# Optimization experiments

Hardware: AMD Instinct MI355X
Metric: run time of the kernel (lower is better)

## Reference

```python
import jax, jax.numpy as jnp
import numpy as np

N = 2048
DIM = 1024
NH = 16
DK = DIM // NH  # 64

def setup_inputs() -> dict:
    key = jax.random.key(0)
    kx, kq, kk, kv = jax.random.split(key, 4)
    # nn.Linear(dim_in, dim_in, bias=False): init ~ U(-1/sqrt(dim_in), 1/sqrt(dim_in))
    b = 1.0 / np.sqrt(DIM)
    return {
        "x": jax.random.normal(kx, (N, DIM), dtype=jnp.float32),
        "rela": jnp.zeros((1,), dtype=jnp.float32),  # unused by the module
        "Wq": jax.random.uniform(kq, (DIM, DIM), jnp.float32, -b, b),
        "Wk": jax.random.uniform(kk, (DIM, DIM), jnp.float32, -b, b),
        "Wv": jax.random.uniform(kv, (DIM, DIM), jnp.float32, -b, b),
    }

def reference(x, rela, Wq, Wk, Wv):
    n = x.shape[0]
    scale = 1.0 / np.sqrt(DK)
    # torch Linear: x @ W.T ; reshape to [n, nh, dk] then heads first -> [nh, n, dk]
    q = (x @ Wq.T).reshape(n, NH, DK).transpose(1, 0, 2)
    k = (x @ Wk.T).reshape(n, NH, DK).transpose(1, 0, 2)
    v = (x @ Wv.T).reshape(n, NH, DK).transpose(1, 0, 2)
    dist = jnp.einsum('hnd,hmd->hnm', q, k) * scale  # [nh, n, n]
    dist = jax.nn.softmax(dist, axis=-1)
    att = jnp.einsum('hnm,hmd->hnd', dist, v)        # [nh, n, dk]
    return att.transpose(1, 0, 2).reshape(n, DIM)
```

## Files before the change

### kernel.cpp

```cpp
#include <hip/hip_runtime.h>

#define SN 2048
#define SDIM 1024
#define SNH 16
#define SDK 64

typedef short short8 __attribute__((ext_vector_type(8)));
typedef short s16x4 __attribute__((ext_vector_type(4)));
typedef unsigned short u16;
typedef u16 u16x4 __attribute__((ext_vector_type(4)));
typedef float f32x4 __attribute__((ext_vector_type(4)));

__device__ __forceinline__ u16 f2b(float f){
  unsigned u = __builtin_bit_cast(unsigned, f);
  u += 0x7fffu + ((u >> 16) & 1u);
  return (u16)(u >> 16);
}

__device__ __forceinline__ float b2f(u16 b){
  unsigned u = ((unsigned)b) << 16;
  return __builtin_bit_cast(float, u);
}

__device__ __forceinline__ float fast_exp2(float x){
#if __has_builtin(__builtin_amdgcn_exp2f)
  return __builtin_amdgcn_exp2f(x);
#else
  float r; asm("v_exp_f32 %0, %1" : "=v"(r) : "v"(x)); return r;
#endif
}

__device__ __forceinline__ f32x4 mfma16(s16x4 a, s16x4 b, f32x4 c){
#if __has_builtin(__builtin_amdgcn_mfma_f32_16x16x16_bf16)
  return __builtin_amdgcn_mfma_f32_16x16x16_bf16(a, b, c, 0, 0, 0);
#elif __has_builtin(__builtin_amdgcn_mfma_f32_16x16x16bf16_1k)
  return __builtin_amdgcn_mfma_f32_16x16x16bf16_1k(a, b, c, 0, 0, 0);
#else
  asm volatile("v_mfma_f32_16x16x16_bf16 %0, %1, %2, %0" : "+v"(c) : "v"(a), "v"(b));
  return c;
#endif
}

__device__ __forceinline__ void async_cp16(const void* g, void* l){
  __builtin_amdgcn_global_load_lds(
      (const __attribute__((address_space(1))) unsigned*)g,
      (__attribute__((address_space(3))) unsigned*)l, 16, 0, 0);
}

__global__ void conv_all(const float* __restrict__ x, const float* __restrict__ wq,
                         const float* __restrict__ wk, const float* __restrict__ wv,
                         u16* __restrict__ xb, u16* __restrict__ wb){
  const int NX4 = (SN * SDIM) / 4;
  const int NW4 = (SDIM * SDIM) / 4;
  const int total = NX4 + 3 * NW4;
  int i = blockIdx.x * blockDim.x + threadIdx.x;
  int stride = gridDim.x * blockDim.x;
  for (int idx = i; idx < total; idx += stride){
    const float* src; u16* dst; int off;
    if (idx < NX4){ src = x; dst = xb; off = idx; }
    else {
      int t = idx - NX4; int ws = t >> 18; off = t & (NW4 - 1);
      src = (ws == 0) ? wq : ((ws == 1) ? wk : wv);
      dst = wb + (size_t)ws * SDIM * SDIM;
    }
    float4 v = reinterpret_cast<const float4*>(src)[off];
    u16x4 o = { f2b(v.x), f2b(v.y), f2b(v.z), f2b(v.w) };
    *reinterpret_cast<u16x4*>(&dst[(size_t)off * 4]) = o;
  }
}

__global__ __launch_bounds__(256) void proj_gemm(const u16* __restrict__ xb, const u16* __restrict__ wb,
                                                 u16* __restrict__ qb, u16* __restrict__ kb,
                                                 u16* __restrict__ vtb){
  __shared__ __align__(16) u16 Asm[2][64 * 64];
  __shared__ __align__(16) u16 Bsm[2][128 * 64];
  const int tid = threadIdx.x, w = tid >> 6, lane = tid & 63;
  const int r = lane & 15, hi = lane >> 4;
  const int tm = blockIdx.x * 64, tn = blockIdx.y * 128;
  const int z = blockIdx.z;
  const u16* W = wb + (size_t)z * SDIM * SDIM;
  const int wr = w >> 1, wc = w & 1;
  const int srow = lane >> 3;
  const int schunk = (lane & 7) ^ (lane >> 3);
  f32x4 acc[2][4] = {};

  auto stage = [&](int b, int kt){
#pragma unroll
    for (int c = 0; c < 2; c++){
      int row = w * 16 + c * 8;
      async_cp16(xb + (size_t)(tm + row + srow) * SDIM + kt + schunk * 8, &Asm[b][row * 64]);
    }
#pragma unroll
    for (int c = 0; c < 4; c++){
      int row = w * 32 + c * 8;
      async_cp16(W + (size_t)(tn + row + srow) * SDIM + kt + schunk * 8, &Bsm[b][row * 64]);
    }
  };

  stage(0, 0);
  asm volatile("s_waitcnt vmcnt(0)" ::: "memory");
  __builtin_amdgcn_s_barrier();
  __builtin_amdgcn_sched_barrier(0);

  int cur = 0;
  for (int kt = 0; kt < SDIM; kt += 64){
    if (kt + 64 < SDIM) stage(cur ^ 1, kt + 64);
    __builtin_amdgcn_s_setprio(1);
#pragma unroll
    for (int kk = 0; kk < 2; kk++){
      short8 af[2], bf[4];
      int cc = (kk * 4 + hi) ^ (r & 7);
#pragma unroll
      for (int mr = 0; mr < 2; mr++)
        af[mr] = *reinterpret_cast<const short8*>(&Asm[cur][(wr * 32 + mr * 16 + r) * 64 + cc * 8]);
#pragma unroll
      for (int nr = 0; nr < 4; nr++)
        bf[nr] = *reinterpret_cast<const short8*>(&Bsm[cur][(wc * 64 + nr * 16 + r) * 64 + cc * 8]);
#pragma unroll
      for (int mr = 0; mr < 2; mr++)
#pragma unroll
        for (int nr = 0; nr < 4; nr++)
          acc[mr][nr] = __builtin_amdgcn_mfma_f32_16x16x32_bf16(af[mr], bf[nr], acc[mr][nr], 0, 0, 0);
    }
    __builtin_amdgcn_s_setprio(0);
    asm volatile("s_waitcnt vmcnt(0)" ::: "memory");
    __builtin_amdgcn_s_barrier();
    __builtin_amdgcn_sched_barrier(0);
    cur ^= 1;
  }

  if (z == 2){
#pragma unroll
    for (int mr = 0; mr < 2; mr++)
#pragma unroll
      for (int nr = 0; nr < 4; nr++){
        u16x4 o4 = { f2b(acc[mr][nr][0]), f2b(acc[mr][nr][1]),
                     f2b(acc[mr][nr][2]), f2b(acc[mr][nr][3]) };
        int col = tn + wc * 64 + nr * 16 + r;
        int row = tm + wr * 32 + mr * 16 + hi * 4;
        *reinterpret_cast<u16x4*>(&vtb[(size_t)col * SN + row]) = o4;
      }
  } else {
    u16* outp = (z == 0) ? qb : kb;
    const float scl = (z == 0) ? 0.18033688011112043f : 1.0f;
#pragma unroll
    for (int mr = 0; mr < 2; mr++)
#pragma unroll
      for (int nr = 0; nr < 4; nr++)
#pragma unroll
        for (int j = 0; j < 4; j++){
          int row = tm + wr * 32 + mr * 16 + hi * 4 + j;
          int col = tn + wc * 64 + nr * 16 + r;
          outp[(size_t)row * SDIM + col] = f2b(acc[mr][nr][j] * scl);
        }
  }
}

__global__ __launch_bounds__(256) void attn(const u16* __restrict__ qb, const u16* __restrict__ kb,
                                            const u16* __restrict__ vtb,
                                            u16* __restrict__ po, float* __restrict__ pl){
  __shared__ __align__(16) u16 klds[2][64 * 64];
  __shared__ __align__(16) u16 vlds[2][64 * 64];
  const int tid = threadIdx.x, w = tid >> 6, lane = tid & 63;
  const int r = lane & 15, hi = lane >> 4;

  int flat = blockIdx.x + 32 * blockIdx.y + 512 * blockIdx.z;
  int sw = (flat & 7) * 256 + (flat >> 3);
  const int q0 = (sw & 31) * 64, h = (sw >> 5) & 15, z = sw >> 9;

  const int srow_off = lane >> 3;
  const int schunk   = (lane & 7) ^ (lane >> 3);

  short8 aq0, aq1;
  {
    int qrow = q0 + w * 16 + r;
    aq0 = *reinterpret_cast<const short8*>(&qb[(size_t)qrow * SDIM + h * SDK + hi * 8]);
    aq1 = *reinterpret_cast<const short8*>(&qb[(size_t)qrow * SDIM + h * SDK + 32 + hi * 8]);
  }
  f32x4 oacc[4] = {};
  float lacc = 0.f;

  auto stage = [&](int b, int t){
#pragma unroll
    for (int c = 0; c < 2; c++){
      int row = w * 16 + c * 8 + srow_off;
      async_cp16(kb  + (size_t)(t + row) * SDIM + h * SDK + schunk * 8,
                 &klds[b][(w * 16 + c * 8) * 64]);
      async_cp16(vtb + (size_t)(h * SDK + row) * SN + t + schunk * 8,
                 &vlds[b][(w * 16 + c * 8) * 64]);
    }
  };

  const int t0 = z * (SN / 4), tend = t0 + (SN / 4);
  stage(0, t0);
  asm volatile("s_waitcnt vmcnt(0)" ::: "memory");
  __builtin_amdgcn_s_barrier();
  __builtin_amdgcn_sched_barrier(0);

  int cur = 0;
  for (int t = t0; t < tend; t += 64){
    if (t + 64 < tend) stage(cur ^ 1, t + 64);

    const u16* kbuf = &klds[cur][0];
    const u16* vbuf = &vlds[cur][0];

    s16x4 bv[4][4];
#pragma unroll
    for (int dt = 0; dt < 4; dt++){
      int row = dt * 16 + r;
      int swz = row & 7;
#pragma unroll
      for (int ct = 0; ct < 4; ct++){
        int chunk = (2 * ct + (hi >> 1)) ^ swz;
        bv[dt][ct] = *reinterpret_cast<const s16x4*>(&vbuf[row * 64 + chunk * 8 + (hi & 1) * 4]);
      }
    }

    f32x4 s[4];
    __builtin_amdgcn_s_setprio(1);
#pragma unroll
    for (int ct = 0; ct < 4; ct++){
      int row = ct * 16 + r;
      int c0 = hi ^ (r & 7);
      short8 bk0 = *reinterpret_cast<const short8*>(&kbuf[row * 64 + c0 * 8]);
      short8 bk1 = *reinterpret_cast<const short8*>(&kbuf[row * 64 + (c0 ^ 4) * 8]);
      f32x4 zero = {};
      s[ct] = __builtin_amdgcn_mfma_f32_16x16x32_bf16(bk0, aq0, zero, 0, 0, 0);
      s[ct] = __builtin_amdgcn_mfma_f32_16x16x32_bf16(bk1, aq1, s[ct], 0, 0, 0);
    }
    __builtin_amdgcn_s_setprio(0);

    s16x4 pa[4];
#pragma unroll
    for (int ct = 0; ct < 4; ct++){
      float p0 = fast_exp2(s[ct][0]), p1 = fast_exp2(s[ct][1]);
      float p2 = fast_exp2(s[ct][2]), p3 = fast_exp2(s[ct][3]);
      lacc += (p0 + p1) + (p2 + p3);
      unsigned d0 = (__builtin_bit_cast(unsigned, p0) >> 16) |
                    (__builtin_bit_cast(unsigned, p1) & 0xffff0000u);
      unsigned d1 = (__builtin_bit_cast(unsigned, p2) >> 16) |
                    (__builtin_bit_cast(unsigned, p3) & 0xffff0000u);
      uint2 dd = { d0, d1 };
      pa[ct] = __builtin_bit_cast(s16x4, dd);
    }

    __builtin_amdgcn_s_setprio(1);
#pragma unroll
    for (int dt = 0; dt < 4; dt++)
#pragma unroll
      for (int ct = 0; ct < 4; ct++)
        oacc[dt] = mfma16(pa[ct], bv[dt][ct], oacc[dt]);
    __builtin_amdgcn_s_setprio(0);

    asm volatile("s_waitcnt vmcnt(0)" ::: "memory");
    __builtin_amdgcn_s_barrier();
    __builtin_amdgcn_sched_barrier(0);
    cur ^= 1;
  }

  lacc += __shfl_xor(lacc, 16);
  lacc += __shfl_xor(lacc, 32);

  const size_t zh = (size_t)z * SNH + h;
#pragma unroll
  for (int dt = 0; dt < 4; dt++)
#pragma unroll
    for (int j = 0; j < 4; j++){
      int row = q0 + w * 16 + hi * 4 + j;
      po[(zh * SN + row) * SDK + dt * 16 + r] = f2b(oacc[dt][j]);
    }
  if (hi == 0)
    pl[zh * SN + q0 + w * 16 + r] = lacc;
}

__global__ void merge(const u16* __restrict__ po, const float* __restrict__ pl,
                      float* __restrict__ out){
  int gid = blockIdx.x * blockDim.x + threadIdx.x;
  int c4 = gid & 15;
  int rowid = gid >> 4;
  int h = rowid & 15, q = rowid >> 4;
  float L = 0.f;
  float4 o = { 0.f, 0.f, 0.f, 0.f };
#pragma unroll
  for (int z = 0; z < 4; z++){
    size_t zh = (size_t)z * SNH + h;
    L += pl[zh * SN + q];
    u16x4 a = *reinterpret_cast<const u16x4*>(&po[(zh * SN + q) * SDK + c4 * 4]);
    o.x += b2f(a[0]); o.y += b2f(a[1]); o.z += b2f(a[2]); o.w += b2f(a[3]);
  }
  float rL = 1.0f / L;
  o.x *= rL; o.y *= rL; o.z *= rL; o.w *= rL;
  reinterpret_cast<float4*>(&out[(size_t)q * SDIM + h * SDK])[c4] = o;
}

extern "C" void kernel_launch(void* const* d_in, const int* in_sizes, int n_in,
                              void* d_out, int out_size, void* d_ws, size_t ws_size,
                              hipStream_t stream){
  const float* x  = (const float*)d_in[0];
  const float* Wq = (const float*)d_in[2];
  const float* Wk = (const float*)d_in[3];
  const float* Wv = (const float*)d_in[4];
  float* out = (float*)d_out;

  char* ws = (char*)d_ws;
  u16* xb  = (u16*)(ws);
  u16* wb  = (u16*)(ws + (4  << 20));
  u16* qb  = (u16*)(ws + (10 << 20));
  u16* kb  = (u16*)(ws + (14 << 20));
  u16* vtb = (u16*)(ws + (18 << 20));
  u16* po  = (u16*)(ws + (22 << 20));
  float* pl = (float*)(ws + (38 << 20));

  conv_all<<<2048, 256, 0, stream>>>(x, Wq, Wk, Wv, xb, wb);

  dim3 pg(SN / 64, SDIM / 128, 3);
  proj_gemm<<<pg, 256, 0, stream>>>(xb, wb, qb, kb, vtb);

  dim3 ag(SN / 64, SNH, 4);
  attn<<<ag, 256, 0, stream>>>(qb, kb, vtb, po, pl);

  merge<<<(SN * SNH * 16) / 256, 256, 0, stream>>>(po, pl, out);
}
```

Baseline: 65.27 us.

## Double query rows per attention wave and use 8 waves in projection GEMM

The attention kernel now has each wave handle 32 query rows (two 16-row sub-tiles), so each K and V tile loaded into shared memory serves twice as many queries and the grid is halved. V fragments are loaded per dt just before use instead of all at once, and an occupancy hint of 4 blocks is added to hold register pressure down. The projection GEMM goes from 4 to 8 waves per block, with each wave computing a 32x32 sub-tile, which adds latency hiding but gives less register-level reuse per wave. The attention change raises register use and leaves fewer blocks to fill the GPU.

```diff
diff --git a/kernel.cpp b/kernel.cpp
--- a/kernel.cpp
+++ b/kernel.cpp
@@ -69,7 +69,7 @@
   }
 }
 
-__global__ __launch_bounds__(256) void proj_gemm(const u16* __restrict__ xb, const u16* __restrict__ wb,
+__global__ __launch_bounds__(512) void proj_gemm(const u16* __restrict__ xb, const u16* __restrict__ wb,
                                                  u16* __restrict__ qb, u16* __restrict__ kb,
                                                  u16* __restrict__ vtb){
   __shared__ __align__(16) u16 Asm[2][64 * 64];
@@ -79,20 +79,16 @@
   const int tm = blockIdx.x * 64, tn = blockIdx.y * 128;
   const int z = blockIdx.z;
   const u16* W = wb + (size_t)z * SDIM * SDIM;
-  const int wr = w >> 1, wc = w & 1;
+  const int wr = w >> 2, wc = w & 3;
   const int srow = lane >> 3;
   const int schunk = (lane & 7) ^ (lane >> 3);
-  f32x4 acc[2][4] = {};
+  f32x4 acc[2][2] = {};
 
   auto stage = [&](int b, int kt){
+    async_cp16(xb + (size_t)(tm + w * 8 + srow) * SDIM + kt + schunk * 8, &Asm[b][w * 8 * 64]);
 #pragma unroll
     for (int c = 0; c < 2; c++){
       int row = w * 16 + c * 8;
-      async_cp16(xb + (size_t)(tm + row + srow) * SDIM + kt + schunk * 8, &Asm[b][row * 64]);
-    }
-#pragma unroll
-    for (int c = 0; c < 4; c++){
-      int row = w * 32 + c * 8;
       async_cp16(W + (size_t)(tn + row + srow) * SDIM + kt + schunk * 8, &Bsm[b][row * 64]);
     }
   };
@@ -108,18 +104,18 @@
     __builtin_amdgcn_s_setprio(1);
 #pragma unroll
     for (int kk = 0; kk < 2; kk++){
-      short8 af[2], bf[4];
+      short8 af[2], bf[2];
       int cc = (kk * 4 + hi) ^ (r & 7);
 #pragma unroll
       for (int mr = 0; mr < 2; mr++)
         af[mr] = *reinterpret_cast<const short8*>(&Asm[cur][(wr * 32 + mr * 16 + r) * 64 + cc * 8]);
 #pragma unroll
-      for (int nr = 0; nr < 4; nr++)
-        bf[nr] = *reinterpret_cast<const short8*>(&Bsm[cur][(wc * 64 + nr * 16 + r) * 64 + cc * 8]);
+      for (int nr = 0; nr < 2; nr++)
+        bf[nr] = *reinterpret_cast<const short8*>(&Bsm[cur][(wc * 32 + nr * 16 + r) * 64 + cc * 8]);
 #pragma unroll
       for (int mr = 0; mr < 2; mr++)
 #pragma unroll
-        for (int nr = 0; nr < 4; nr++)
+        for (int nr = 0; nr < 2; nr++)
           acc[mr][nr] = __builtin_amdgcn_mfma_f32_16x16x32_bf16(af[mr], bf[nr], acc[mr][nr], 0, 0, 0);
     }
     __builtin_amdgcn_s_setprio(0);
@@ -133,10 +129,10 @@
 #pragma unroll
     for (int mr = 0; mr < 2; mr++)
 #pragma unroll
-      for (int nr = 0; nr < 4; nr++){
+      for (int nr = 0; nr < 2; nr++){
         u16x4 o4 = { f2b(acc[mr][nr][0]), f2b(acc[mr][nr][1]),
                      f2b(acc[mr][nr][2]), f2b(acc[mr][nr][3]) };
-        int col = tn + wc * 64 + nr * 16 + r;
+        int col = tn + wc * 32 + nr * 16 + r;
         int row = tm + wr * 32 + mr * 16 + hi * 4;
         *reinterpret_cast<u16x4*>(&vtb[(size_t)col * SN + row]) = o4;
       }
@@ -146,39 +142,40 @@
 #pragma unroll
     for (int mr = 0; mr < 2; mr++)
 #pragma unroll
-      for (int nr = 0; nr < 4; nr++)
+      for (int nr = 0; nr < 2; nr++)
 #pragma unroll
         for (int j = 0; j < 4; j++){
           int row = tm + wr * 32 + mr * 16 + hi * 4 + j;
-          int col = tn + wc * 64 + nr * 16 + r;
+          int col = tn + wc * 32 + nr * 16 + r;
           outp[(size_t)row * SDIM + col] = f2b(acc[mr][nr][j] * scl);
         }
   }
 }
 
-__global__ __launch_bounds__(256) void attn(const u16* __restrict__ qb, const u16* __restrict__ kb,
-                                            const u16* __restrict__ vtb,
-                                            u16* __restrict__ po, float* __restrict__ pl){
+__global__ __launch_bounds__(256, 4) void attn(const u16* __restrict__ qb, const u16* __restrict__ kb,
+                                               const u16* __restrict__ vtb,
+                                               u16* __restrict__ po, float* __restrict__ pl){
   __shared__ __align__(16) u16 klds[2][64 * 64];
   __shared__ __align__(16) u16 vlds[2][64 * 64];
   const int tid = threadIdx.x, w = tid >> 6, lane = tid & 63;
   const int r = lane & 15, hi = lane >> 4;
 
-  int flat = blockIdx.x + 32 * blockIdx.y + 512 * blockIdx.z;
-  int sw = (flat & 7) * 256 + (flat >> 3);
-  const int q0 = (sw & 31) * 64, h = (sw >> 5) & 15, z = sw >> 9;
+  int flat = blockIdx.x + 16 * blockIdx.y + 256 * blockIdx.z;
+  int sw = (flat & 7) * 128 + (flat >> 3);
+  const int q0 = (sw & 15) * 128, h = (sw >> 4) & 15, z = sw >> 8;
 
   const int srow_off = lane >> 3;
   const int schunk   = (lane & 7) ^ (lane >> 3);
 
-  short8 aq0, aq1;
-  {
-    int qrow = q0 + w * 16 + r;
-    aq0 = *reinterpret_cast<const short8*>(&qb[(size_t)qrow * SDIM + h * SDK + hi * 8]);
-    aq1 = *reinterpret_cast<const short8*>(&qb[(size_t)qrow * SDIM + h * SDK + 32 + hi * 8]);
-  }
-  f32x4 oacc[4] = {};
-  float lacc = 0.f;
+  short8 aq[2][2];
+#pragma unroll
+  for (int sub = 0; sub < 2; sub++){
+    int qrow = q0 + w * 32 + sub * 16 + r;
+    aq[sub][0] = *reinterpret_cast<const short8*>(&qb[(size_t)qrow * SDIM + h * SDK + hi * 8]);
+    aq[sub][1] = *reinterpret_cast<const short8*>(&qb[(size_t)qrow * SDIM + h * SDK + 32 + hi * 8]);
+  }
+  f32x4 oacc[2][4] = {};
+  float lacc0 = 0.f, lacc1 = 0.f;
 
   auto stage = [&](int b, int t){
 #pragma unroll
@@ -204,19 +201,7 @@
     const u16* kbuf = &klds[cur][0];
     const u16* vbuf = &vlds[cur][0];
 
-    s16x4 bv[4][4];
-#pragma unroll
-    for (int dt = 0; dt < 4; dt++){
-      int row = dt * 16 + r;
-      int swz = row & 7;
-#pragma unroll
-      for (int ct = 0; ct < 4; ct++){
-        int chunk = (2 * ct + (hi >> 1)) ^ swz;
-        bv[dt][ct] = *reinterpret_cast<const s16x4*>(&vbuf[row * 64 + chunk * 8 + (hi & 1) * 4]);
-      }
-    }
-
-    f32x4 s[4];
+    f32x4 s0[4], s1[4];
     __builtin_amdgcn_s_setprio(1);
 #pragma unroll
     for (int ct = 0; ct < 4; ct++){
@@ -225,31 +210,53 @@
       short8 bk0 = *reinterpret_cast<const short8*>(&kbuf[row * 64 + c0 * 8]);
       short8 bk1 = *reinterpret_cast<const short8*>(&kbuf[row * 64 + (c0 ^ 4) * 8]);
       f32x4 zero = {};
-      s[ct] = __builtin_amdgcn_mfma_f32_16x16x32_bf16(bk0, aq0, zero, 0, 0, 0);
-      s[ct] = __builtin_amdgcn_mfma_f32_16x16x32_bf16(bk1, aq1, s[ct], 0, 0, 0);
+      s0[ct] = __builtin_amdgcn_mfma_f32_16x16x32_bf16(bk0, aq[0][0], zero, 0, 0, 0);
+      s1[ct] = __builtin_amdgcn_mfma_f32_16x16x32_bf16(bk0, aq[1][0], zero, 0, 0, 0);
+      s0[ct] = __builtin_amdgcn_mfma_f32_16x16x32_bf16(bk1, aq[0][1], s0[ct], 0, 0, 0);
+      s1[ct] = __builtin_amdgcn_mfma_f32_16x16x32_bf16(bk1, aq[1][1], s1[ct], 0, 0, 0);
     }
     __builtin_amdgcn_s_setprio(0);
 
-    s16x4 pa[4];
+    s16x4 pa0[4], pa1[4];
 #pragma unroll
     for (int ct = 0; ct < 4; ct++){
-      float p0 = fast_exp2(s[ct][0]), p1 = fast_exp2(s[ct][1]);
-      float p2 = fast_exp2(s[ct][2]), p3 = fast_exp2(s[ct][3]);
-      lacc += (p0 + p1) + (p2 + p3);
-      unsigned d0 = (__builtin_bit_cast(unsigned, p0) >> 16) |
-                    (__builtin_bit_cast(unsigned, p1) & 0xffff0000u);
-      unsigned d1 = (__builtin_bit_cast(unsigned, p2) >> 16) |
-                    (__builtin_bit_cast(unsigned, p3) & 0xffff0000u);
-      uint2 dd = { d0, d1 };
-      pa[ct] = __builtin_bit_cast(s16x4, dd);
+      float a0 = fast_exp2(s0[ct][0]), a1 = fast_exp2(s0[ct][1]);
+      float a2 = fast_exp2(s0[ct][2]), a3 = fast_exp2(s0[ct][3]);
+      lacc0 += (a0 + a1) + (a2 + a3);
+      unsigned d0 = (__builtin_bit_cast(unsigned, a0) >> 16) |
+                    (__builtin_bit_cast(unsigned, a1) & 0xffff0000u);
+      unsigned d1 = (__builtin_bit_cast(unsigned, a2) >> 16) |
+                    (__builtin_bit_cast(unsigned, a3) & 0xffff0000u);
+      uint2 dd0 = { d0, d1 };
+      pa0[ct] = __builtin_bit_cast(s16x4, dd0);
+      float b0 = fast_exp2(s1[ct][0]), b1 = fast_exp2(s1[ct][1]);
+      float b2 = fast_exp2(s1[ct][2]), b3 = fast_exp2(s1[ct][3]);
+      lacc1 += (b0 + b1) + (b2 + b3);
+      unsigned e0 = (__builtin_bit_cast(unsigned, b0) >> 16) |
+                    (__builtin_bit_cast(unsigned, b1) & 0xffff0000u);
+      unsigned e1 = (__builtin_bit_cast(unsigned, b2) >> 16) |
+                    (__builtin_bit_cast(unsigned, b3) & 0xffff0000u);
+      uint2 dd1 = { e0, e1 };
+      pa1[ct] = __builtin_bit_cast(s16x4, dd1);
     }
 
     __builtin_amdgcn_s_setprio(1);
 #pragma unroll
-    for (int dt = 0; dt < 4; dt++)
-#pragma unroll
-      for (int ct = 0; ct < 4; ct++)
-        oacc[dt] = mfma16(pa[ct], bv[dt][ct], oacc[dt]);
+    for (int dt = 0; dt < 4; dt++){
+      int row = dt * 16 + r;
+      int swz = row & 7;
+      s16x4 bvd[4];
+#pragma unroll
+      for (int ct = 0; ct < 4; ct++){
+        int chunk = (2 * ct + (hi >> 1)) ^ swz;
+        bvd[ct] = *reinterpret_cast<const s16x4*>(&vbuf[row * 64 + chunk * 8 + (hi & 1) * 4]);
+      }
+#pragma unroll
+      for (int ct = 0; ct < 4; ct++){
+        oacc[0][dt] = mfma16(pa0[ct], bvd[ct], oacc[0][dt]);
+        oacc[1][dt] = mfma16(pa1[ct], bvd[ct], oacc[1][dt]);
+      }
+    }
     __builtin_amdgcn_s_setprio(0);
 
     asm volatile("s_waitcnt vmcnt(0)" ::: "memory");
@@ -258,19 +265,23 @@
     cur ^= 1;
   }
 
-  lacc += __shfl_xor(lacc, 16);
-  lacc += __shfl_xor(lacc, 32);
+  lacc0 += __shfl_xor(lacc0, 16); lacc0 += __shfl_xor(lacc0, 32);
+  lacc1 += __shfl_xor(lacc1, 16); lacc1 += __shfl_xor(lacc1, 32);
 
   const size_t zh = (size_t)z * SNH + h;
 #pragma unroll
-  for (int dt = 0; dt < 4; dt++)
-#pragma unroll
-    for (int j = 0; j < 4; j++){
-      int row = q0 + w * 16 + hi * 4 + j;
-      po[(zh * SN + row) * SDK + dt * 16 + r] = f2b(oacc[dt][j]);
-    }
-  if (hi == 0)
-    pl[zh * SN + q0 + w * 16 + r] = lacc;
+  for (int sub = 0; sub < 2; sub++)
+#pragma unroll
+    for (int dt = 0; dt < 4; dt++)
+#pragma unroll
+      for (int j = 0; j < 4; j++){
+        int row = q0 + w * 32 + sub * 16 + hi * 4 + j;
+        po[(zh * SN + row) * SDK + dt * 16 + r] = f2b(oacc[sub][dt][j]);
+      }
+  if (hi == 0){
+    pl[zh * SN + q0 + w * 32 + r] = lacc0;
+    pl[zh * SN + q0 + w * 32 + 16 + r] = lacc1;
+  }
 }
 
 __global__ void merge(const u16* __restrict__ po, const float* __restrict__ pl,
@@ -314,9 +325,9 @@
   conv_all<<<2048, 256, 0, stream>>>(x, Wq, Wk, Wv, xb, wb);
 
   dim3 pg(SN / 64, SDIM / 128, 3);
-  proj_gemm<<<pg, 256, 0, stream>>>(xb, wb, qb, kb, vtb);
-
-  dim3 ag(SN / 64, SNH, 4);
+  proj_gemm<<<pg, 512, 0, stream>>>(xb, wb, qb, kb, vtb);
+
+  dim3 ag(SN / 128, SNH, 4);
   attn<<<ag, 256, 0, stream>>>(qb, kb, vtb, po, pl);
 
   merge<<<(SN * SNH * 16) / 256, 256, 0, stream>>>(po, pl, out);
```

New measurement: 60.78 us. 1.07x faster.
